# Performance work log

Measured on AMD Instinct MI355X. Metric: run time of the kernel, lower is better.

The kernel has to match this reference:

```python
import jax, jax.numpy as jnp
import numpy as np

EPS = 1e-5


def _layernorm(x, w, b):
    mu = jnp.mean(x, axis=-1, keepdims=True)
    var = jnp.var(x, axis=-1, keepdims=True)
    return (x - mu) * jax.lax.rsqrt(var + EPS) * w + b


def setup_inputs() -> dict:
    key = jax.random.key(0)
    ks = jax.random.split(key, 3)
    h, dff = 1024, 4096
    x = jax.random.normal(ks[0], (4, 2048, h), dtype=jnp.float32)
    w1 = jax.random.normal(ks[1], (h, dff), dtype=jnp.float32) * (1.0 / np.sqrt(h))
    w2 = jax.random.normal(ks[2], (dff, h), dtype=jnp.float32) * (1.0 / np.sqrt(dff))
    return {
        "x": x,
        "ln1_w": jnp.ones((h,), jnp.float32),
        "ln1_b": jnp.zeros((h,), jnp.float32),
        "ln2_w": jnp.ones((h,), jnp.float32),
        "ln2_b": jnp.zeros((h,), jnp.float32),
        "w1": w1,
        "b1": jnp.zeros((dff,), jnp.float32),
        "w2": w2,
        "b2": jnp.zeros((h,), jnp.float32),
    }


def reference(x, ln1_w, ln1_b, ln2_w, ln2_b, w1, b1, w2, b2):
    # double 1D FFT: over hidden (dim=-1) then sequence (dim=-2), keep real part
    fourier_x = jnp.fft.fft(jnp.fft.fft(x, axis=-1), axis=-2).real
    x = x + fourier_x
    x = _layernorm(x, ln1_w, ln1_b)
    # FFN: Linear -> exact GELU -> Linear (dropout is identity in eval)
    h = jax.nn.gelu(jnp.einsum("bsd,df->bsf", x, w1) + b1, approximate=False)
    x = x + jnp.einsum("bsf,fd->bsd", h, w2) + b2
    return _layernorm(x, ln2_w, ln2_b)
```

## Files before the change

### kernel.cpp

```cpp
#include <hip/hip_runtime.h>
#include <hip/hip_bf16.h>
#include <math.h>

typedef __bf16 bf16_t;
typedef __bf16 bf16x8 __attribute__((ext_vector_type(8)));
typedef __bf16 bf16x4 __attribute__((ext_vector_type(4)));
typedef float  f32x4  __attribute__((ext_vector_type(4)));

#define NROWS 8192
#define HD    1024
#define DFF   4096
#define HKEEP 513

typedef __attribute__((address_space(1))) const void* gas_cptr;
typedef __attribute__((address_space(3))) void* las_ptr;

__device__ __forceinline__ void gload_lds16(const void* g, void* l) {
  __builtin_amdgcn_global_load_lds((gas_cptr)g, (las_ptr)l, 16, 0, 0);
}

template <int N> __device__ __forceinline__ void vmw() {
  if      constexpr (N==4)  asm volatile("s_waitcnt vmcnt(4)"  ::: "memory");
  else if constexpr (N==6)  asm volatile("s_waitcnt vmcnt(6)"  ::: "memory");
}

__global__ __launch_bounds__(256) void transpose_to_bf16(
    const float* __restrict__ in, bf16_t* __restrict__ out, int R, int C)
{
  __shared__ float tile[32][33];
  const int bx = blockIdx.x, by = blockIdx.y;
  const int tx = threadIdx.x, ty = threadIdx.y;
  #pragma unroll
  for (int i = ty; i < 32; i += 8)
    tile[i][tx] = in[(size_t)(by*32 + i)*C + bx*32 + tx];
  __syncthreads();
  #pragma unroll
  for (int i = ty; i < 32; i += 8)
    out[(size_t)(bx*32 + i)*R + by*32 + tx] = (bf16_t)tile[tx][i];
}

#define RPB 16
#define LDW 1036
__global__ __launch_bounds__(512) void fft_h_t(
    const float* __restrict__ x, float* __restrict__ reT, float* __restrict__ imT)
{
  __shared__ float sre[RPB*LDW], sim[RPB*LDW], twc[512], tws[512];
  const int t = threadIdx.x;
  const int row0 = blockIdx.x * RPB;
  {
    float sv, cv; sincosf(-6.28318530717958647692f * (float)t * (1.0f/1024.0f), &sv, &cv);
    twc[t] = cv; tws[t] = sv;
  }
  #pragma unroll
  for (int q = 0; q < 8; ++q) {
    const int i = t + 512*q;
    const int row = i >> 8, c4 = i & 255;
    float4 v = *(const float4*)(x + (size_t)(row0+row)*HD + c4*4);
    *(float4*)&sre[row*LDW + c4*4] = v;
  }
  __syncthreads();
  const int b0i = __brev((unsigned)t) >> 22;
  const int b1i = __brev((unsigned)(t + 512)) >> 22;
  float rv[32];
  #pragma unroll
  for (int q = 0; q < 16; ++q) {
    rv[2*q]   = sre[q*LDW + b0i];
    rv[2*q+1] = sre[q*LDW + b1i];
  }
  __syncthreads();
  #pragma unroll
  for (int q = 0; q < 16; ++q) {
    sre[q*LDW + t]       = rv[2*q];
    sre[q*LDW + t + 512] = rv[2*q+1];
    sim[q*LDW + t]       = 0.0f;
    sim[q*LDW + t + 512] = 0.0f;
  }
  __syncthreads();
  for (int s = 0; s < 10; ++s) {
    const int half = 1 << s;
    const int j    = t & (half - 1);
    const int ib   = ((t >> s) << (s + 1)) | j;
    const int ti2  = j << (9 - s);
    const float wc = twc[ti2], ws = tws[ti2];
    #pragma unroll
    for (int q = 0; q < 16; ++q) {
      float* pr = &sre[q*LDW]; float* pi = &sim[q*LDW];
      const float r1 = pr[ib],      i1v = pi[ib];
      const float r2 = pr[ib+half], i2v = pi[ib+half];
      const float tr = r2*wc - i2v*ws;
      const float ti = r2*ws + i2v*wc;
      pr[ib]      = r1 + tr; pi[ib]      = i1v + ti;
      pr[ib+half] = r1 - tr; pi[ib+half] = i1v - ti;
    }
    __syncthreads();
  }
  const int tx = t & 15, th = t >> 4;
  #pragma unroll
  for (int hh = 0; hh < 17; ++hh) {
    const int h = hh*32 + th;
    if (h < HKEEP) {
      reT[(size_t)h*NROWS + row0 + tx] = sre[tx*LDW + h];
      imT[(size_t)h*NROWS + row0 + tx] = sim[tx*LDW + h];
    }
  }
}

__global__ __launch_bounds__(256) void fft_s_col(
    const float* __restrict__ reT, const float* __restrict__ imT,
    float* __restrict__ fT)
{
  __shared__ float sre[2048], sim[2048], twc[1024], tws[1024];
  const int t = threadIdx.x;
  const int h = blockIdx.x;
  const int batch = blockIdx.y;
  const size_t base = (size_t)h * NROWS + batch * 2048;
  for (int k = t; k < 1024; k += 256) {
    float sv, cv; sincosf(-6.28318530717958647692f * (float)k * (1.0f/2048.0f), &sv, &cv);
    twc[k] = cv; tws[k] = sv;
  }
  #pragma unroll
  for (int q = 0; q < 8; ++q) {
    const int i = t + 256*q;
    const int src = __brev((unsigned)i) >> 21;
    sre[i] = reT[base + src];
    sim[i] = imT[base + src];
  }
  __syncthreads();
  for (int s = 0; s < 11; ++s) {
    const int half = 1 << s;
    #pragma unroll
    for (int q = 0; q < 4; ++q) {
      const int b  = t + 256*q;
      const int j  = b & (half - 1);
      const int ib = ((b >> s) << (s + 1)) | j;
      const int ti2 = j << (10 - s);
      const float wc = twc[ti2], ws = tws[ti2];
      const float r1 = sre[ib],       i1v = sim[ib];
      const float r2 = sre[ib+half],  i2v = sim[ib+half];
      const float tr = r2*wc - i2v*ws;
      const float ti = r2*ws + i2v*wc;
      sre[ib]      = r1 + tr; sim[ib]      = i1v + ti;
      sre[ib+half] = r1 - tr; sim[ib+half] = i1v - ti;
    }
    __syncthreads();
  }
  #pragma unroll
  for (int q = 0; q < 8; ++q) {
    const int i = t + 256*q;
    fT[base + i] = sre[i];
  }
}

__global__ __launch_bounds__(256) void umadd_kernel(
    const float* __restrict__ fT, const float* __restrict__ x,
    float* __restrict__ y)
{
  __shared__ float tile[32][33];
  const int h0 = blockIdx.x * 32;
  const int b0 = blockIdx.y * 32;
  const int tx = threadIdx.x, ty = threadIdx.y;
  const int batch = b0 >> 11;
  const int s0    = b0 & 2047;
  #pragma unroll
  for (int i = ty; i < 32; i += 8) {
    const int h = h0 + i;
    float v;
    if (h <= 512) {
      v = fT[(size_t)h * NROWS + b0 + tx];
    } else {
      const int sp = (2048 - (s0 + tx)) & 2047;
      v = fT[(size_t)(1024 - h) * NROWS + (batch << 11) + sp];
    }
    tile[i][tx] = v;
  }
  __syncthreads();
  #pragma unroll
  for (int i = ty; i < 32; i += 8) {
    const size_t gi = (size_t)(b0+i)*HD + h0+tx;
    y[gi] = x[gi] + tile[tx][i];
  }
}

template <bool OUT_BF16>
__global__ __launch_bounds__(256) void layernorm_k(
    const float* __restrict__ in, const float* __restrict__ gw,
    const float* __restrict__ gb, bf16_t* __restrict__ ob, float* __restrict__ of)
{
  __shared__ float red[8];
  const size_t row = blockIdx.x;
  const int t = threadIdx.x;
  const float* xr = in + row * HD;
  float4 v = *(const float4*)(xr + t*4);
  float s = v.x + v.y + v.z + v.w;
  #pragma unroll
  for (int o = 32; o > 0; o >>= 1) s += __shfl_xor(s, o);
  if ((t & 63) == 0) red[t >> 6] = s;
  __syncthreads();
  const float mu = (red[0]+red[1]+red[2]+red[3]) * (1.0f/1024.0f);
  const float dx = v.x-mu, dy = v.y-mu, dz = v.z-mu, dw = v.w-mu;
  float sq = dx*dx + dy*dy + dz*dz + dw*dw;
  #pragma unroll
  for (int o = 32; o > 0; o >>= 1) sq += __shfl_xor(sq, o);
  if ((t & 63) == 0) red[4 + (t >> 6)] = sq;
  __syncthreads();
  const float var  = (red[4]+red[5]+red[6]+red[7]) * (1.0f/1024.0f);
  const float rstd = rsqrtf(var + 1e-5f);
  const float4 wv = *(const float4*)(gw + t*4);
  const float4 bv = *(const float4*)(gb + t*4);
  const float o0 = dx*rstd*wv.x + bv.x;
  const float o1 = dy*rstd*wv.y + bv.y;
  const float o2 = dz*rstd*wv.z + bv.z;
  const float o3 = dw*rstd*wv.w + bv.w;
  if constexpr (OUT_BF16) {
    bf16x4 o; o[0]=(bf16_t)o0; o[1]=(bf16_t)o1; o[2]=(bf16_t)o2; o[3]=(bf16_t)o3;
    *(bf16x4*)(ob + row*HD + t*4) = o;
  } else {
    float4 o; o.x=o0; o.y=o1; o.z=o2; o.w=o3;
    *(float4*)(of + row*HD + t*4) = o;
  }
}

__device__ __forceinline__ float gelu_fast(float v) {
  const float u  = 0.7978845608028654f * v * (1.0f + 0.044715f * v * v);
  const float e  = exp2f(-2.8853900817779268f * u);
  return v / (1.0f + e);
}

template <int NQ, bool GELU_OUT>
__global__ __launch_bounds__(512, 2) void gemm8r(
    const bf16_t* __restrict__ A,
    const bf16_t* __restrict__ Bt,
    const float*  __restrict__ bias,
    const bf16_t* __restrict__ resid,
    bf16_t* __restrict__ outB, float* __restrict__ outF,
    int M, int N, int K, int gx)
{
  __shared__ bf16_t As[2][2][128*64];
  __shared__ bf16_t Bs[2][2][NQ*64*64];

  const int tid  = threadIdx.x;
  const int wave = tid >> 6, lane = tid & 63;
  const int wr = wave >> 2, wc = wave & 3;
  const int lr = lane & 15, lkg = lane >> 4;

  const int nwg = gridDim.x;
  const int sid = (blockIdx.x & 7) * (nwg >> 3) + (blockIdx.x >> 3);
  const int bx = sid % gx, by = sid / gx;
  const int brow = by * 256, bcol = bx * (NQ*128);

  const int rl = lane >> 3;
  const int sg = (lane & 7) ^ rl;

  auto stageA = [&](int b, int mh, int tt) {
    #pragma unroll
    for (int l = 0; l < 2; ++l) {
      const int row = brow + l*128 + mh*64 + wave*8 + rl;
      gload_lds16(A + (size_t)row * K + tt*64 + sg*8,
                  &As[b][mh][(l*64 + wave*8)*64]);
    }
  };
  auto stageB = [&](int b, int nh, int tt) {
    #pragma unroll
    for (int l = 0; l < NQ; ++l) {
      const int rho = l*64 + wave*8 + rl;
      const int wcs = rho / (NQ*16), r = rho % (NQ*16);
      const int row = bcol + wcs*(NQ*32) + nh*(NQ*16) + r;
      gload_lds16(Bt + (size_t)row * K + tt*64 + sg*8,
                  &Bs[b][nh][(l*64 + wave*8)*64]);
    }
  };

  f32x4 acc[8][2*NQ] = {};
  bf16x8 af[4][2];
  bf16x8 bq[2][NQ][2];

  const int NT = K >> 6;
  const int NI = NT >> 1;
  constexpr int WT = (NQ==2) ? 6 : 4;

  #define PHASE(BUF, MH, NH, DOA, DOB, STG, DOW) do { \
    if constexpr (DOA) { \
      _Pragma("unroll") for (int m = 0; m < 4; ++m) { \
      _Pragma("unroll") for (int ks = 0; ks < 2; ++ks) \
        af[m][ks] = *(const bf16x8*)&As[BUF][MH][(wr*64 + m*16 + lr)*64 + (((lkg + ks*4) ^ (lr & 7)) << 3)]; } \
    } \
    if constexpr (DOB) { \
      _Pragma("unroll") for (int n = 0; n < NQ; ++n) { \
      _Pragma("unroll") for (int ks = 0; ks < 2; ++ks) \
        bq[NH][n][ks] = *(const bf16x8*)&Bs[BUF][NH][(wc*(NQ*16) + n*16 + lr)*64 + (((lkg + ks*4) ^ (lr & 7)) << 3)]; } \
    } \
    STG; \
    __builtin_amdgcn_s_barrier(); \
    asm volatile("s_waitcnt lgkmcnt(0)" ::: "memory"); \
    __builtin_amdgcn_sched_barrier(0); \
    __builtin_amdgcn_s_setprio(1); \
    _Pragma("unroll") for (int m = 0; m < 4; ++m) { \
    _Pragma("unroll") for (int n = 0; n < NQ; ++n) { \
    _Pragma("unroll") for (int ks = 0; ks < 2; ++ks) \
      acc[(MH)*4+m][(NH)*NQ+n] = __builtin_amdgcn_mfma_f32_16x16x32_bf16(bq[NH][n][ks], af[m][ks], acc[(MH)*4+m][(NH)*NQ+n], 0, 0, 0); } } \
    __builtin_amdgcn_s_setprio(0); \
    if constexpr (DOW) vmw<WT>(); \
    __builtin_amdgcn_s_barrier(); \
  } while (0)

  stageB(0,0,0); stageA(0,0,0); stageB(0,1,0); stageA(0,1,0);
  stageB(1,0,1); stageA(1,0,1); stageB(1,1,1);
  vmw<WT>();
  __builtin_amdgcn_s_barrier();

  for (int j = 0; j < NI; ++j) {
    const int c1 = 2*j + 1;
    const int n2 = (2*j + 2 < NT) ? 2*j + 2 : NT - 1;
    const int n3 = (2*j + 3 < NT) ? 2*j + 3 : NT - 1;
    PHASE(0, 0, 0, 1, 1, stageA(1,1,c1), false);
    PHASE(0, 0, 1, 0, 1, stageB(0,0,n2), false);
    PHASE(0, 1, 1, 1, 0, stageA(0,0,n2), false);
    PHASE(0, 1, 0, 0, 0, stageB(0,1,n2), true);
    PHASE(1, 0, 0, 1, 1, stageA(0,1,n2), false);
    PHASE(1, 0, 1, 0, 1, stageB(1,0,n3), false);
    PHASE(1, 1, 1, 1, 0, stageA(1,0,n3), false);
    PHASE(1, 1, 0, 0, 0, stageB(1,1,n3), true);
  }
  #undef PHASE

  #pragma unroll
  for (int im = 0; im < 8; ++im) {
    const int row = brow + wr*128 + (im >> 2)*64 + (im & 3)*16 + lr;
    #pragma unroll
    for (int in = 0; in < 2*NQ; ++in) {
      const int col = bcol + wc*(NQ*32) + (in/NQ)*(NQ*16) + (in%NQ)*16 + lkg*4;
      const float4 bv4 = *(const float4*)(bias + col);
      float v0 = acc[im][in][0] + bv4.x;
      float v1 = acc[im][in][1] + bv4.y;
      float v2 = acc[im][in][2] + bv4.z;
      float v3 = acc[im][in][3] + bv4.w;
      if constexpr (GELU_OUT) {
        bf16x4 o;
        o[0] = (bf16_t)gelu_fast(v0); o[1] = (bf16_t)gelu_fast(v1);
        o[2] = (bf16_t)gelu_fast(v2); o[3] = (bf16_t)gelu_fast(v3);
        *(bf16x4*)(outB + (size_t)row * N + col) = o;
      } else {
        bf16x4 rr = *(const bf16x4*)(resid + (size_t)row * N + col);
        float4 o;
        o.x = v0 + (float)rr[0]; o.y = v1 + (float)rr[1];
        o.z = v2 + (float)rr[2]; o.w = v3 + (float)rr[3];
        *(float4*)(outF + (size_t)row * N + col) = o;
      }
    }
  }
}

extern "C" void kernel_launch(void* const* d_in, const int* in_sizes, int n_in,
                              void* d_out, int out_size, void* d_ws, size_t ws_size,
                              hipStream_t stream) {
  const float* x    = (const float*)d_in[0];
  const float* ln1w = (const float*)d_in[1];
  const float* ln1b = (const float*)d_in[2];
  const float* ln2w = (const float*)d_in[3];
  const float* ln2b = (const float*)d_in[4];
  const float* w1   = (const float*)d_in[5];
  const float* b1   = (const float*)d_in[6];
  const float* w2   = (const float*)d_in[7];
  const float* b2   = (const float*)d_in[8];
  float* out = (float*)d_out;

  char* ws = (char*)d_ws;
  bf16_t* w1b = (bf16_t*)(ws);
  bf16_t* w2b = (bf16_t*)(ws + (8u   << 20));
  float*  reT = (float*) (ws + (16u  << 20));
  float*  imT = (float*) (ws + (33u  << 20));
  float*  fT  = (float*) (ws + (50u  << 20));
  float*  y   = (float*) (ws + (67u  << 20));
  bf16_t* xn  = (bf16_t*)(ws + (99u  << 20));
  bf16_t* hg  = (bf16_t*)(ws + (16u  << 20));

  transpose_to_bf16<<<dim3(DFF/32, HD/32), dim3(32, 8), 0, stream>>>(w1, w1b, HD, DFF);
  transpose_to_bf16<<<dim3(HD/32, DFF/32), dim3(32, 8), 0, stream>>>(w2, w2b, DFF, HD);

  fft_h_t<<<NROWS/RPB, 512, 0, stream>>>(x, reT, imT);

  fft_s_col<<<dim3(513, 4), 256, 0, stream>>>(reT, imT, fT);

  umadd_kernel<<<dim3(HD/32, NROWS/32), dim3(32, 8), 0, stream>>>(fT, x, y);

  layernorm_k<true><<<NROWS, 256, 0, stream>>>(y, ln1w, ln1b, xn, nullptr);

  gemm8r<2, true><<<(NROWS/256)*(DFF/256), 512, 0, stream>>>(
      xn, w1b, b1, nullptr, hg, nullptr, NROWS, DFF, HD, DFF/256);
  gemm8r<1, false><<<(NROWS/256)*(HD/128), 512, 0, stream>>>(
      hg, w2b, b2, xn, nullptr, out, NROWS, HD, DFF, HD/128);

  layernorm_k<false><<<NROWS, 256, 0, stream>>>(out, ln2w, ln2b, nullptr, out);
}
```

Before: 311.1 us.

## Pack row pairs into one complex FFT and keep GEMM2 output in bf16

The hidden-dim FFT now packs two real rows into a single complex 1024-point FFT, as real and imaginary parts. The two spectra are separated afterwards using conjugate symmetry, which halves the butterfly work and shared memory per block. Separately, the second GEMM writes its residual-added output as bf16 to a scratch buffer, and the final layernorm reads bf16 and writes fp32. This cuts the intermediate traffic but loses some precision before the last normalization.

```diff
diff --git a/kernel.cpp b/kernel.cpp
--- a/kernel.cpp
+++ b/kernel.cpp
@@ -44,7 +44,7 @@
 __global__ __launch_bounds__(512) void fft_h_t(
     const float* __restrict__ x, float* __restrict__ reT, float* __restrict__ imT)
 {
-  __shared__ float sre[RPB*LDW], sim[RPB*LDW], twc[512], tws[512];
+  __shared__ float sre[8*LDW], sim[8*LDW], twc[512], tws[512];
   const int t = threadIdx.x;
   const int row0 = blockIdx.x * RPB;
   {
@@ -52,28 +52,33 @@
     twc[t] = cv; tws[t] = sv;
   }
   #pragma unroll
-  for (int q = 0; q < 8; ++q) {
+  for (int q = 0; q < 4; ++q) {
     const int i = t + 512*q;
-    const int row = i >> 8, c4 = i & 255;
-    float4 v = *(const float4*)(x + (size_t)(row0+row)*HD + c4*4);
-    *(float4*)&sre[row*LDW + c4*4] = v;
+    const int pr = i >> 8;
+    const int c4 = i & 255;
+    float4 vr = *(const float4*)(x + (size_t)(row0 + 2*pr    )*HD + c4*4);
+    float4 vi = *(const float4*)(x + (size_t)(row0 + 2*pr + 1)*HD + c4*4);
+    *(float4*)&sre[pr*LDW + c4*4] = vr;
+    *(float4*)&sim[pr*LDW + c4*4] = vi;
   }
   __syncthreads();
   const int b0i = __brev((unsigned)t) >> 22;
   const int b1i = __brev((unsigned)(t + 512)) >> 22;
   float rv[32];
   #pragma unroll
-  for (int q = 0; q < 16; ++q) {
-    rv[2*q]   = sre[q*LDW + b0i];
-    rv[2*q+1] = sre[q*LDW + b1i];
-  }
-  __syncthreads();
-  #pragma unroll
-  for (int q = 0; q < 16; ++q) {
-    sre[q*LDW + t]       = rv[2*q];
-    sre[q*LDW + t + 512] = rv[2*q+1];
-    sim[q*LDW + t]       = 0.0f;
-    sim[q*LDW + t + 512] = 0.0f;
+  for (int q = 0; q < 8; ++q) {
+    rv[4*q]   = sre[q*LDW + b0i];
+    rv[4*q+1] = sre[q*LDW + b1i];
+    rv[4*q+2] = sim[q*LDW + b0i];
+    rv[4*q+3] = sim[q*LDW + b1i];
+  }
+  __syncthreads();
+  #pragma unroll
+  for (int q = 0; q < 8; ++q) {
+    sre[q*LDW + t]       = rv[4*q];
+    sre[q*LDW + t + 512] = rv[4*q+1];
+    sim[q*LDW + t]       = rv[4*q+2];
+    sim[q*LDW + t + 512] = rv[4*q+3];
   }
   __syncthreads();
   for (int s = 0; s < 10; ++s) {
@@ -83,7 +88,7 @@
     const int ti2  = j << (9 - s);
     const float wc = twc[ti2], ws = tws[ti2];
     #pragma unroll
-    for (int q = 0; q < 16; ++q) {
+    for (int q = 0; q < 8; ++q) {
       float* pr = &sre[q*LDW]; float* pi = &sim[q*LDW];
       const float r1 = pr[ib],      i1v = pi[ib];
       const float r2 = pr[ib+half], i2v = pi[ib+half];
@@ -95,12 +100,19 @@
     __syncthreads();
   }
   const int tx = t & 15, th = t >> 4;
+  const int q  = tx >> 1, par = tx & 1;
   #pragma unroll
   for (int hh = 0; hh < 17; ++hh) {
     const int h = hh*32 + th;
     if (h < HKEEP) {
-      reT[(size_t)h*NROWS + row0 + tx] = sre[tx*LDW + h];
-      imT[(size_t)h*NROWS + row0 + tx] = sim[tx*LDW + h];
+      const int mh = (1024 - h) & 1023;
+      const float zr = sre[q*LDW + h],  zi = sim[q*LDW + h];
+      const float mr = sre[q*LDW + mh], mi = sim[q*LDW + mh];
+      float orr, oii;
+      if (par == 0) { orr = 0.5f*(zr + mr); oii = 0.5f*(zi - mi); }
+      else          { orr = 0.5f*(zi + mi); oii = 0.5f*(mr - zr); }
+      reT[(size_t)h*NROWS + row0 + tx] = orr;
+      imT[(size_t)h*NROWS + row0 + tx] = oii;
     }
   }
 }
@@ -181,10 +193,9 @@
   }
 }
 
-template <bool OUT_BF16>
-__global__ __launch_bounds__(256) void layernorm_k(
+__global__ __launch_bounds__(256) void layernorm_f2b(
     const float* __restrict__ in, const float* __restrict__ gw,
-    const float* __restrict__ gb, bf16_t* __restrict__ ob, float* __restrict__ of)
+    const float* __restrict__ gb, bf16_t* __restrict__ ob)
 {
   __shared__ float red[8];
   const size_t row = blockIdx.x;
@@ -207,17 +218,45 @@
   const float rstd = rsqrtf(var + 1e-5f);
   const float4 wv = *(const float4*)(gw + t*4);
   const float4 bv = *(const float4*)(gb + t*4);
-  const float o0 = dx*rstd*wv.x + bv.x;
-  const float o1 = dy*rstd*wv.y + bv.y;
-  const float o2 = dz*rstd*wv.z + bv.z;
-  const float o3 = dw*rstd*wv.w + bv.w;
-  if constexpr (OUT_BF16) {
-    bf16x4 o; o[0]=(bf16_t)o0; o[1]=(bf16_t)o1; o[2]=(bf16_t)o2; o[3]=(bf16_t)o3;
-    *(bf16x4*)(ob + row*HD + t*4) = o;
-  } else {
-    float4 o; o.x=o0; o.y=o1; o.z=o2; o.w=o3;
-    *(float4*)(of + row*HD + t*4) = o;
-  }
+  bf16x4 o;
+  o[0] = (bf16_t)(dx*rstd*wv.x + bv.x);
+  o[1] = (bf16_t)(dy*rstd*wv.y + bv.y);
+  o[2] = (bf16_t)(dz*rstd*wv.z + bv.z);
+  o[3] = (bf16_t)(dw*rstd*wv.w + bv.w);
+  *(bf16x4*)(ob + row*HD + t*4) = o;
+}
+
+__global__ __launch_bounds__(256) void layernorm_b2f(
+    const bf16_t* __restrict__ in, const float* __restrict__ gw,
+    const float* __restrict__ gb, float* __restrict__ of)
+{
+  __shared__ float red[8];
+  const size_t row = blockIdx.x;
+  const int t = threadIdx.x;
+  bf16x4 v4 = *(const bf16x4*)(in + row*HD + t*4);
+  const float vx = (float)v4[0], vy = (float)v4[1], vz = (float)v4[2], vw = (float)v4[3];
+  float s = vx + vy + vz + vw;
+  #pragma unroll
+  for (int o = 32; o > 0; o >>= 1) s += __shfl_xor(s, o);
+  if ((t & 63) == 0) red[t >> 6] = s;
+  __syncthreads();
+  const float mu = (red[0]+red[1]+red[2]+red[3]) * (1.0f/1024.0f);
+  const float dx = vx-mu, dy = vy-mu, dz = vz-mu, dw = vw-mu;
+  float sq = dx*dx + dy*dy + dz*dz + dw*dw;
+  #pragma unroll
+  for (int o = 32; o > 0; o >>= 1) sq += __shfl_xor(sq, o);
+  if ((t & 63) == 0) red[4 + (t >> 6)] = sq;
+  __syncthreads();
+  const float var  = (red[4]+red[5]+red[6]+red[7]) * (1.0f/1024.0f);
+  const float rstd = rsqrtf(var + 1e-5f);
+  const float4 wv = *(const float4*)(gw + t*4);
+  const float4 bv = *(const float4*)(gb + t*4);
+  float4 o;
+  o.x = dx*rstd*wv.x + bv.x;
+  o.y = dy*rstd*wv.y + bv.y;
+  o.z = dz*rstd*wv.z + bv.z;
+  o.w = dw*rstd*wv.w + bv.w;
+  *(float4*)(of + row*HD + t*4) = o;
 }
 
 __device__ __forceinline__ float gelu_fast(float v) {
@@ -232,7 +271,7 @@
     const bf16_t* __restrict__ Bt,
     const float*  __restrict__ bias,
     const bf16_t* __restrict__ resid,
-    bf16_t* __restrict__ outB, float* __restrict__ outF,
+    bf16_t* __restrict__ outB,
     int M, int N, int K, int gx)
 {
   __shared__ bf16_t As[2][2][128*64];
@@ -334,18 +373,16 @@
       float v1 = acc[im][in][1] + bv4.y;
       float v2 = acc[im][in][2] + bv4.z;
       float v3 = acc[im][in][3] + bv4.w;
+      bf16x4 o;
       if constexpr (GELU_OUT) {
-        bf16x4 o;
         o[0] = (bf16_t)gelu_fast(v0); o[1] = (bf16_t)gelu_fast(v1);
         o[2] = (bf16_t)gelu_fast(v2); o[3] = (bf16_t)gelu_fast(v3);
-        *(bf16x4*)(outB + (size_t)row * N + col) = o;
       } else {
         bf16x4 rr = *(const bf16x4*)(resid + (size_t)row * N + col);
-        float4 o;
-        o.x = v0 + (float)rr[0]; o.y = v1 + (float)rr[1];
-        o.z = v2 + (float)rr[2]; o.w = v3 + (float)rr[3];
-        *(float4*)(outF + (size_t)row * N + col) = o;
+        o[0] = (bf16_t)(v0 + (float)rr[0]); o[1] = (bf16_t)(v1 + (float)rr[1]);
+        o[2] = (bf16_t)(v2 + (float)rr[2]); o[3] = (bf16_t)(v3 + (float)rr[3]);
       }
+      *(bf16x4*)(outB + (size_t)row * N + col) = o;
     }
   }
 }
@@ -373,6 +410,7 @@
   float*  y   = (float*) (ws + (67u  << 20));
   bf16_t* xn  = (bf16_t*)(ws + (99u  << 20));
   bf16_t* hg  = (bf16_t*)(ws + (16u  << 20));
+  bf16_t* z   = (bf16_t*)(ws + (80u  << 20));
 
   transpose_to_bf16<<<dim3(DFF/32, HD/32), dim3(32, 8), 0, stream>>>(w1, w1b, HD, DFF);
   transpose_to_bf16<<<dim3(HD/32, DFF/32), dim3(32, 8), 0, stream>>>(w2, w2b, DFF, HD);
@@ -383,12 +421,12 @@
 
   umadd_kernel<<<dim3(HD/32, NROWS/32), dim3(32, 8), 0, stream>>>(fT, x, y);
 
-  layernorm_k<true><<<NROWS, 256, 0, stream>>>(y, ln1w, ln1b, xn, nullptr);
+  layernorm_f2b<<<NROWS, 256, 0, stream>>>(y, ln1w, ln1b, xn);
 
   gemm8r<2, true><<<(NROWS/256)*(DFF/256), 512, 0, stream>>>(
-      xn, w1b, b1, nullptr, hg, nullptr, NROWS, DFF, HD, DFF/256);
+      xn, w1b, b1, nullptr, hg, NROWS, DFF, HD, DFF/256);
   gemm8r<1, false><<<(NROWS/256)*(HD/128), 512, 0, stream>>>(
-      hg, w2b, b2, xn, nullptr, out, NROWS, HD, DFF, HD/128);
-
-  layernorm_k<false><<<NROWS, 256, 0, stream>>>(out, ln2w, ln2b, nullptr, out);
-}
+      hg, w2b, b2, xn, z, NROWS, HD, DFF, HD/128);
+
+  layernorm_b2f<<<NROWS, 256, 0, stream>>>(z, ln2w, ln2b, out);
+}
```

New measurement: 286.9 us. 1.08x faster.
